# Optimization experiments

Hardware: AMD Instinct MI355X
Metric: run time of the kernel (lower is better)

## Reference

```python
import jax, jax.numpy as jnp
import numpy as np

ALPHA = 0.2  # LeakyReLU negative slope
NEG_INF = -9e15


def setup_inputs() -> dict:
    key = jax.random.key(0)
    k1, k2, k3, k4 = jax.random.split(key, 4)
    N, F_IN, F_OUT = 8192, 128, 64
    h = jax.random.normal(k1, (N, F_IN), dtype=jnp.float32)
    adj = jax.random.randint(k2, (N, N), 0, 2, dtype=jnp.int32)
    # xavier_uniform with gain=1.414 (as in the torch module)
    gain = 1.414
    bW = gain * np.sqrt(6.0 / (F_IN + F_OUT))
    W = jax.random.uniform(k3, (F_IN, F_OUT), dtype=jnp.float32, minval=-bW, maxval=bW)
    ba = gain * np.sqrt(6.0 / (2 * F_OUT + 1))
    a = jax.random.uniform(k4, (2 * F_OUT, 1), dtype=jnp.float32, minval=-ba, maxval=ba)
    return {"h": h, "adj": adj, "W": W, "a": a}


def reference(h, adj, W, a):
    # Wh: [N, F_out]
    Wh = h @ W
    F_out = Wh.shape[1]
    # Decompose a^T [Wh_i || Wh_j] = (Wh @ a_src)_i + (Wh @ a_dst)_j
    # (same math as the repeat+concat construction, without the N*N*2F tensor)
    src = Wh @ a[:F_out, 0]   # [N]
    dst = Wh @ a[F_out:, 0]   # [N]
    e = jax.nn.leaky_relu(src[:, None] + dst[None, :], negative_slope=ALPHA)  # [N, N]
    e = jnp.where(adj > 0, e, jnp.float32(NEG_INF))
    attention = jax.nn.softmax(e, axis=1)  # [N, N]
    h_prime = attention @ Wh               # [N, F_out]
    return jax.nn.elu(h_prime)
```

## Files before the change

### kernel.cpp

```cpp
#include <hip/hip_runtime.h>

#define ALPHA 0.2f
#define NN 8192
#define FIN 128
#define FOUT 64

typedef short bf16x8 __attribute__((ext_vector_type(8)));
typedef float f32x4 __attribute__((ext_vector_type(4)));

__device__ __forceinline__ unsigned short f2b(float x) {
    unsigned u = __builtin_bit_cast(unsigned, x);
    unsigned r = (u + 0x7fffu + ((u >> 16) & 1u)) >> 16;
    return (unsigned short)r;
}

__global__ __launch_bounds__(256) void gat_k0(const int* __restrict__ adj,
                                              unsigned long long* __restrict__ adjb) {
    int t = threadIdx.x, w = t >> 6, l = t & 63;
    int row = blockIdx.x * 4 + w;
    const int4* a4 = (const int4*)(adj + (size_t)row * NN);
    unsigned long long* ob = adjb + (size_t)row * 32 * 4;
#pragma unroll 4
    for (int it = 0; it < 32; ++it) {
        int4 av = a4[it * 64 + l];
        unsigned long long b0 = __ballot(av.x != 0);
        unsigned long long b1 = __ballot(av.y != 0);
        unsigned long long b2 = __ballot(av.z != 0);
        unsigned long long b3 = __ballot(av.w != 0);
        if (l == 0) {
            ulonglong4 v;
            v.x = b0; v.y = b1; v.z = b2; v.w = b3;
            *(ulonglong4*)(ob + it * 4) = v;
        }
    }
}

__global__ __launch_bounds__(256) void gat_k1(const float* __restrict__ h,
                                              const float* __restrict__ W,
                                              const float* __restrict__ a,
                                              float* __restrict__ Wh,
                                              float* __restrict__ src,
                                              float* __restrict__ dst) {
    __shared__ float wlds[FIN * FOUT];
    int t = threadIdx.x;
    const float4* W4 = (const float4*)W;
    float4* wlds4 = (float4*)wlds;
#pragma unroll
    for (int q = 0; q < 8; ++q) wlds4[q * 256 + t] = W4[q * 256 + t];
    __syncthreads();
    int wave = t >> 6, lane = t & 63;
    int row = blockIdx.x * 4 + wave;
    const float4* h4 = (const float4*)(h + (size_t)row * FIN);
    float acc = 0.f;
#pragma unroll
    for (int k4 = 0; k4 < 32; ++k4) {
        float4 hv = h4[k4];
        acc = fmaf(hv.x, wlds[(k4 * 4 + 0) * 64 + lane], acc);
        acc = fmaf(hv.y, wlds[(k4 * 4 + 1) * 64 + lane], acc);
        acc = fmaf(hv.z, wlds[(k4 * 4 + 2) * 64 + lane], acc);
        acc = fmaf(hv.w, wlds[(k4 * 4 + 3) * 64 + lane], acc);
    }
    Wh[(size_t)row * 64 + lane] = acc;
    float sa = acc * a[lane];
    float da = acc * a[64 + lane];
#pragma unroll
    for (int off = 32; off; off >>= 1) {
        sa += __shfl_xor(sa, off);
        da += __shfl_xor(da, off);
    }
    if (lane == 0) { src[row] = sa; dst[row] = da; }
}

__global__ __launch_bounds__(256) void gat_k1b(const float* __restrict__ Wh,
                                               unsigned short* __restrict__ whbt) {
    __shared__ unsigned short t16[64 * 68];
    int t = threadIdx.x;
    int rb = blockIdx.x * 64;
    const float4* s4 = (const float4*)(Wh + (size_t)rb * 64);
#pragma unroll
    for (int q = 0; q < 4; ++q) {
        float4 v = s4[t * 4 + q];
        int flat = t * 16 + q * 4;
        int r = flat >> 6, f = flat & 63;
        unsigned short* p = &t16[r * 68 + f];
        p[0] = f2b(v.x); p[1] = f2b(v.y); p[2] = f2b(v.z); p[3] = f2b(v.w);
    }
    __syncthreads();
    int f = t >> 2, qr = t & 3;
    unsigned v[8];
#pragma unroll
    for (int k = 0; k < 8; ++k) {
        unsigned lo = t16[(qr * 16 + 2 * k + 0) * 68 + f];
        unsigned hi = t16[(qr * 16 + 2 * k + 1) * 68 + f];
        v[k] = lo | (hi << 16);
    }
    uint4* o = (uint4*)(whbt + (size_t)f * NN + rb + qr * 16);
    o[0] = make_uint4(v[0], v[1], v[2], v[3]);
    o[1] = make_uint4(v[4], v[5], v[6], v[7]);
}

__global__ __launch_bounds__(256) void gat_k2(const unsigned long long* __restrict__ adjb,
                                              const unsigned short* __restrict__ whbt,
                                              const float* __restrict__ src,
                                              const float* __restrict__ dst,
                                              float* __restrict__ pl,
                                              float* __restrict__ pacc,
                                              int ns, int js) {
    const int l = threadIdx.x & 63;
    const int w = threadIdx.x >> 6;
    const int r = l & 15;
    const int g = l >> 4;
    const int s = blockIdx.x;
    const int rg = blockIdx.y;
    const int task = rg * ns + s;
    const int row = rg * 64 + w * 16 + r;
    const int j0 = s * js;

    const float srcv = src[row];
    const float4* dst4 = (const float4*)dst;
    const unsigned long long* brow = adjb + (size_t)row * 32 * 4;

    f32x4 acc0 = {0.f, 0.f, 0.f, 0.f}, acc1 = acc0, acc2 = acc0, acc3 = acc0, accl = acc0;
    bf16x8 bones;
#pragma unroll
    for (int e = 0; e < 8; ++e) bones[e] = (short)0x3F80;

    const int g0 = j0 >> 8, g1 = (j0 + js) >> 8;
    ulonglong2 mA = *(const ulonglong2*)(brow + g0 * 4);
    ulonglong2 mB = *(const ulonglong2*)(brow + g0 * 4 + 2);

    for (int grp = g0; grp < g1; ++grp) {
        int ng = (grp + 1 < g1) ? grp + 1 : g0;
        ulonglong2 nA = *(const ulonglong2*)(brow + ng * 4);
        ulonglong2 nB = *(const ulonglong2*)(brow + ng * 4 + 2);
        unsigned long long m0 = mA.x, m1 = mA.y, m2 = mB.x, m3 = mB.y;
        const int jgrp = grp << 8;
#pragma unroll 2
        for (int hh = 0; hh < 8; ++hh) {
            const int jh = jgrp + hh * 32;
            const int hb = hh * 8 + 2 * g;
            float4 d0 = dst4[(jh >> 2) + 2 * g];
            float4 d1 = dst4[(jh >> 2) + 2 * g + 1];
            float xs[8] = {d0.x, d0.y, d0.z, d0.w, d1.x, d1.y, d1.z, d1.w};
            float p[8];
#pragma unroll
            for (int e = 0; e < 8; ++e) {
                float x = srcv + xs[e];
                float lr = fmaxf(x, 0.f) + ALPHA * fminf(x, 0.f);
                float pe = __expf(lr);
                unsigned long long mm = (e & 3) == 0 ? m0 : (e & 3) == 1 ? m1
                                      : (e & 3) == 2 ? m2 : m3;
                unsigned bit = (unsigned)(mm >> (hb + (e >> 2))) & 1u;
                p[e] = bit ? pe : 0.f;
            }
            unsigned pw0, pw1, pw2, pw3;
            asm("v_cvt_pk_bf16_f32 %0, %1, %2" : "=v"(pw0) : "v"(p[0]), "v"(p[1]));
            asm("v_cvt_pk_bf16_f32 %0, %1, %2" : "=v"(pw1) : "v"(p[2]), "v"(p[3]));
            asm("v_cvt_pk_bf16_f32 %0, %1, %2" : "=v"(pw2) : "v"(p[4]), "v"(p[5]));
            asm("v_cvt_pk_bf16_f32 %0, %1, %2" : "=v"(pw3) : "v"(p[6]), "v"(p[7]));
            uint4 pwv = make_uint4(pw0, pw1, pw2, pw3);
            bf16x8 af = __builtin_bit_cast(bf16x8, pwv);

            const unsigned short* bbase = whbt + (size_t)r * NN + jh + 8 * g;
            bf16x8 b0 = *(const bf16x8*)(bbase + 0 * 16 * NN);
            bf16x8 b1 = *(const bf16x8*)(bbase + 1 * 16 * NN);
            bf16x8 b2 = *(const bf16x8*)(bbase + 2 * 16 * NN);
            bf16x8 b3 = *(const bf16x8*)(bbase + 3 * 16 * NN);
            acc0 = __builtin_amdgcn_mfma_f32_16x16x32_bf16(af, b0, acc0, 0, 0, 0);
            acc1 = __builtin_amdgcn_mfma_f32_16x16x32_bf16(af, b1, acc1, 0, 0, 0);
            acc2 = __builtin_amdgcn_mfma_f32_16x16x32_bf16(af, b2, acc2, 0, 0, 0);
            acc3 = __builtin_amdgcn_mfma_f32_16x16x32_bf16(af, b3, acc3, 0, 0, 0);
            accl = __builtin_amdgcn_mfma_f32_16x16x32_bf16(af, bones, accl, 0, 0, 0);
        }
        mA = nA; mB = nB;
    }

    if (r == 0) {
        float* plo = pl + (size_t)task * 64 + w * 16 + g * 4;
        plo[0] = accl[0]; plo[1] = accl[1]; plo[2] = accl[2]; plo[3] = accl[3];
    }

    float* po = pacc + (size_t)task * 4096 + (size_t)(w * 16) * 64;
#pragma unroll
    for (int reg = 0; reg < 4; ++reg) {
        int m = g * 4 + reg;
        po[m * 64 + 0 * 16 + r] = acc0[reg];
        po[m * 64 + 1 * 16 + r] = acc1[reg];
        po[m * 64 + 2 * 16 + r] = acc2[reg];
        po[m * 64 + 3 * 16 + r] = acc3[reg];
    }
}

__global__ __launch_bounds__(256) void gat_k3(const float* __restrict__ pl,
                                              const float* __restrict__ pacc,
                                              float* __restrict__ out, int ns) {
    int t = threadIdx.x;
    int wave = t >> 6, lane = t & 63;
    int row = blockIdx.x * 4 + wave;
    int rg = row >> 6, rr = row & 63;
    float L = 0.f, o = 0.f;
    for (int s2 = 0; s2 < ns; ++s2) {
        L += pl[(size_t)(rg * ns + s2) * 64 + rr];
        o += pacc[(size_t)(rg * ns + s2) * 4096 + rr * 64 + lane];
    }
    float hp = o / L;
    out[(size_t)row * 64 + lane] = hp > 0.f ? hp : __expf(hp) - 1.f;
}

extern "C" void kernel_launch(void* const* d_in, const int* in_sizes, int n_in,
                              void* d_out, int out_size, void* d_ws, size_t ws_size,
                              hipStream_t stream) {
    const float* h = (const float*)d_in[0];
    const int* adj = (const int*)d_in[1];
    const float* W = (const float*)d_in[2];
    const float* a = (const float*)d_in[3];
    float* out = (float*)d_out;
    float* ws = (float*)d_ws;

    size_t avail = ws_size / sizeof(float);
    int ns = 4;
    while (ns > 1 && (size_t)2899968 + (size_t)ns * 532480 > avail) ns >>= 1;
    int js = NN / ns;

    float* Wh = ws;
    float* src = Wh + (size_t)NN * FOUT;
    float* dst = src + NN;
    float* pl = dst + NN;
    float* pacc = pl + (size_t)128 * ns * 64;
    unsigned short* whbt = (unsigned short*)(pacc + (size_t)128 * ns * 4096);
    unsigned long long* adjb = (unsigned long long*)((float*)whbt + 262144);

    gat_k0<<<dim3(NN / 4), dim3(256), 0, stream>>>(adj, adjb);
    gat_k1<<<dim3(NN / 4), dim3(256), 0, stream>>>(h, W, a, Wh, src, dst);
    gat_k1b<<<dim3(NN / 64), dim3(256), 0, stream>>>(Wh, whbt);
    gat_k2<<<dim3(ns, 128), dim3(256), 0, stream>>>(adjb, whbt, src, dst, pl, pacc, ns, js);
    gat_k3<<<dim3(NN / 4), dim3(256), 0, stream>>>(pl, pacc, out, ns);
}
```

Before: 455.2 us.

## Pre-swizzle bf16 Wh into MFMA fragment layout and prefetch in flattened loop

The Wh transpose kernel now writes bf16 values in the exact per-lane MFMA B-fragment order, so the attention kernel makes one coalesced 16-byte load per lane per step instead of four strided row loads. The main loop is flattened to one 32-column step per iteration and software-prefetches the next step's B fragments and adjacency mask words. The column split count is raised from 4 to 8, and occupancy hints are added. In exchange, the partial-result buffers and the final reduction grow, and register pressure from prefetching rises.

```diff
diff --git a/kernel.cpp b/kernel.cpp
--- a/kernel.cpp
+++ b/kernel.cpp
@@ -7,12 +7,6 @@
 
 typedef short bf16x8 __attribute__((ext_vector_type(8)));
 typedef float f32x4 __attribute__((ext_vector_type(4)));
-
-__device__ __forceinline__ unsigned short f2b(float x) {
-    unsigned u = __builtin_bit_cast(unsigned, x);
-    unsigned r = (u + 0x7fffu + ((u >> 16) & 1u)) >> 16;
-    return (unsigned short)r;
-}
 
 __global__ __launch_bounds__(256) void gat_k0(const int* __restrict__ adj,
                                               unsigned long long* __restrict__ adjb) {
@@ -72,40 +66,33 @@
 }
 
 __global__ __launch_bounds__(256) void gat_k1b(const float* __restrict__ Wh,
-                                               unsigned short* __restrict__ whbt) {
-    __shared__ unsigned short t16[64 * 68];
-    int t = threadIdx.x;
-    int rb = blockIdx.x * 64;
-    const float4* s4 = (const float4*)(Wh + (size_t)rb * 64);
-#pragma unroll
-    for (int q = 0; q < 4; ++q) {
-        float4 v = s4[t * 4 + q];
-        int flat = t * 16 + q * 4;
-        int r = flat >> 6, f = flat & 63;
-        unsigned short* p = &t16[r * 68 + f];
-        p[0] = f2b(v.x); p[1] = f2b(v.y); p[2] = f2b(v.z); p[3] = f2b(v.w);
-    }
+                                               uint4* __restrict__ whbt2) {
+    __shared__ float wt[32 * 64];
+    int tid = threadIdx.x;
+    int t = blockIdx.x;
+    const float4* s4 = (const float4*)(Wh + (size_t)t * 2048);
+    float4* l4 = (float4*)wt;
+    l4[tid] = s4[tid];
+    l4[tid + 256] = s4[tid + 256];
     __syncthreads();
-    int f = t >> 2, qr = t & 3;
-    unsigned v[8];
-#pragma unroll
-    for (int k = 0; k < 8; ++k) {
-        unsigned lo = t16[(qr * 16 + 2 * k + 0) * 68 + f];
-        unsigned hi = t16[(qr * 16 + 2 * k + 1) * 68 + f];
-        v[k] = lo | (hi << 16);
-    }
-    uint4* o = (uint4*)(whbt + (size_t)f * NN + rb + qr * 16);
-    o[0] = make_uint4(v[0], v[1], v[2], v[3]);
-    o[1] = make_uint4(v[4], v[5], v[6], v[7]);
-}
-
-__global__ __launch_bounds__(256) void gat_k2(const unsigned long long* __restrict__ adjb,
-                                              const unsigned short* __restrict__ whbt,
-                                              const float* __restrict__ src,
-                                              const float* __restrict__ dst,
-                                              float* __restrict__ pl,
-                                              float* __restrict__ pacc,
-                                              int ns, int js) {
+    int q = tid >> 6, l = tid & 63, r = l & 15, g = l >> 4;
+    unsigned pk[4];
+#pragma unroll
+    for (int k = 0; k < 4; ++k) {
+        float lo = wt[(8 * g + 2 * k + 0) * 64 + 16 * q + r];
+        float hi = wt[(8 * g + 2 * k + 1) * 64 + 16 * q + r];
+        asm("v_cvt_pk_bf16_f32 %0, %1, %2" : "=v"(pk[k]) : "v"(lo), "v"(hi));
+    }
+    whbt2[(size_t)t * 256 + tid] = make_uint4(pk[0], pk[1], pk[2], pk[3]);
+}
+
+__global__ __launch_bounds__(256, 4) void gat_k2(const unsigned long long* __restrict__ adjb,
+                                                 const uint4* __restrict__ whbt2,
+                                                 const float* __restrict__ src,
+                                                 const float* __restrict__ dst,
+                                                 float* __restrict__ pl,
+                                                 float* __restrict__ pacc,
+                                                 int ns, int js) {
     const int l = threadIdx.x & 63;
     const int w = threadIdx.x >> 6;
     const int r = l & 15;
@@ -115,34 +102,43 @@
     const int task = rg * ns + s;
     const int row = rg * 64 + w * 16 + r;
     const int j0 = s * js;
+    const int steps = js >> 5;
 
     const float srcv = src[row];
     const float4* dst4 = (const float4*)dst;
-    const unsigned long long* brow = adjb + (size_t)row * 32 * 4;
+    const ulonglong2* brow2 = (const ulonglong2*)(adjb + (size_t)row * 128);
+    const uint4* bt = whbt2 + l;
 
     f32x4 acc0 = {0.f, 0.f, 0.f, 0.f}, acc1 = acc0, acc2 = acc0, acc3 = acc0, accl = acc0;
     bf16x8 bones;
 #pragma unroll
     for (int e = 0; e < 8; ++e) bones[e] = (short)0x3F80;
 
-    const int g0 = j0 >> 8, g1 = (j0 + js) >> 8;
-    ulonglong2 mA = *(const ulonglong2*)(brow + g0 * 4);
-    ulonglong2 mB = *(const ulonglong2*)(brow + g0 * 4 + 2);
-
-    for (int grp = g0; grp < g1; ++grp) {
-        int ng = (grp + 1 < g1) ? grp + 1 : g0;
-        ulonglong2 nA = *(const ulonglong2*)(brow + ng * 4);
-        ulonglong2 nB = *(const ulonglong2*)(brow + ng * 4 + 2);
-        unsigned long long m0 = mA.x, m1 = mA.y, m2 = mB.x, m3 = mB.y;
-        const int jgrp = grp << 8;
-#pragma unroll 2
-        for (int hh = 0; hh < 8; ++hh) {
-            const int jh = jgrp + hh * 32;
-            const int hb = hh * 8 + 2 * g;
-            float4 d0 = dst4[(jh >> 2) + 2 * g];
-            float4 d1 = dst4[(jh >> 2) + 2 * g + 1];
+    int jh = j0;
+    uint4 b0 = bt[(jh >> 5) * 256 + 0 * 64];
+    uint4 b1 = bt[(jh >> 5) * 256 + 1 * 64];
+    uint4 b2 = bt[(jh >> 5) * 256 + 2 * 64];
+    uint4 b3 = bt[(jh >> 5) * 256 + 3 * 64];
+    ulonglong2 mA = brow2[(jh >> 8) * 2 + 0];
+    ulonglong2 mB = brow2[(jh >> 8) * 2 + 1];
+
+    for (int t = 0; t < steps; ++t, jh += 32) {
+        const int jn = (t + 1 < steps) ? jh + 32 : j0;
+        uint4 nb0 = bt[(jn >> 5) * 256 + 0 * 64];
+        uint4 nb1 = bt[(jn >> 5) * 256 + 1 * 64];
+        uint4 nb2 = bt[(jn >> 5) * 256 + 2 * 64];
+        uint4 nb3 = bt[(jn >> 5) * 256 + 3 * 64];
+        ulonglong2 nmA = brow2[(jn >> 8) * 2 + 0];
+        ulonglong2 nmB = brow2[(jn >> 8) * 2 + 1];
+
+        float4 d0 = dst4[(jh >> 2) + 2 * g];
+        float4 d1 = dst4[(jh >> 2) + 2 * g + 1];
+        const int hb = ((jh >> 5) & 7) * 8 + 2 * g;
+        const unsigned long long m0 = mA.x, m1 = mA.y, m2 = mB.x, m3 = mB.y;
+
+        float p[8];
+        {
             float xs[8] = {d0.x, d0.y, d0.z, d0.w, d1.x, d1.y, d1.z, d1.w};
-            float p[8];
 #pragma unroll
             for (int e = 0; e < 8; ++e) {
                 float x = srcv + xs[e];
@@ -153,26 +149,22 @@
                 unsigned bit = (unsigned)(mm >> (hb + (e >> 2))) & 1u;
                 p[e] = bit ? pe : 0.f;
             }
-            unsigned pw0, pw1, pw2, pw3;
-            asm("v_cvt_pk_bf16_f32 %0, %1, %2" : "=v"(pw0) : "v"(p[0]), "v"(p[1]));
-            asm("v_cvt_pk_bf16_f32 %0, %1, %2" : "=v"(pw1) : "v"(p[2]), "v"(p[3]));
-            asm("v_cvt_pk_bf16_f32 %0, %1, %2" : "=v"(pw2) : "v"(p[4]), "v"(p[5]));
-            asm("v_cvt_pk_bf16_f32 %0, %1, %2" : "=v"(pw3) : "v"(p[6]), "v"(p[7]));
-            uint4 pwv = make_uint4(pw0, pw1, pw2, pw3);
-            bf16x8 af = __builtin_bit_cast(bf16x8, pwv);
-
-            const unsigned short* bbase = whbt + (size_t)r * NN + jh + 8 * g;
-            bf16x8 b0 = *(const bf16x8*)(bbase + 0 * 16 * NN);
-            bf16x8 b1 = *(const bf16x8*)(bbase + 1 * 16 * NN);
-            bf16x8 b2 = *(const bf16x8*)(bbase + 2 * 16 * NN);
-            bf16x8 b3 = *(const bf16x8*)(bbase + 3 * 16 * NN);
-            acc0 = __builtin_amdgcn_mfma_f32_16x16x32_bf16(af, b0, acc0, 0, 0, 0);
-            acc1 = __builtin_amdgcn_mfma_f32_16x16x32_bf16(af, b1, acc1, 0, 0, 0);
-            acc2 = __builtin_amdgcn_mfma_f32_16x16x32_bf16(af, b2, acc2, 0, 0, 0);
-            acc3 = __builtin_amdgcn_mfma_f32_16x16x32_bf16(af, b3, acc3, 0, 0, 0);
-            accl = __builtin_amdgcn_mfma_f32_16x16x32_bf16(af, bones, accl, 0, 0, 0);
         }
-        mA = nA; mB = nB;
+        unsigned pw0, pw1, pw2, pw3;
+        asm("v_cvt_pk_bf16_f32 %0, %1, %2" : "=v"(pw0) : "v"(p[0]), "v"(p[1]));
+        asm("v_cvt_pk_bf16_f32 %0, %1, %2" : "=v"(pw1) : "v"(p[2]), "v"(p[3]));
+        asm("v_cvt_pk_bf16_f32 %0, %1, %2" : "=v"(pw2) : "v"(p[4]), "v"(p[5]));
+        asm("v_cvt_pk_bf16_f32 %0, %1, %2" : "=v"(pw3) : "v"(p[6]), "v"(p[7]));
+        bf16x8 af = __builtin_bit_cast(bf16x8, make_uint4(pw0, pw1, pw2, pw3));
+
+        acc0 = __builtin_amdgcn_mfma_f32_16x16x32_bf16(af, __builtin_bit_cast(bf16x8, b0), acc0, 0, 0, 0);
+        acc1 = __builtin_amdgcn_mfma_f32_16x16x32_bf16(af, __builtin_bit_cast(bf16x8, b1), acc1, 0, 0, 0);
+        acc2 = __builtin_amdgcn_mfma_f32_16x16x32_bf16(af, __builtin_bit_cast(bf16x8, b2), acc2, 0, 0, 0);
+        acc3 = __builtin_amdgcn_mfma_f32_16x16x32_bf16(af, __builtin_bit_cast(bf16x8, b3), acc3, 0, 0, 0);
+        accl = __builtin_amdgcn_mfma_f32_16x16x32_bf16(af, bones, accl, 0, 0, 0);
+
+        b0 = nb0; b1 = nb1; b2 = nb2; b3 = nb3;
+        mA = nmA; mB = nmB;
     }
 
     if (r == 0) {
@@ -218,7 +210,7 @@
     float* ws = (float*)d_ws;
 
     size_t avail = ws_size / sizeof(float);
-    int ns = 4;
+    int ns = 8;
     while (ns > 1 && (size_t)2899968 + (size_t)ns * 532480 > avail) ns >>= 1;
     int js = NN / ns;
 
@@ -227,12 +219,12 @@
     float* dst = src + NN;
     float* pl = dst + NN;
     float* pacc = pl + (size_t)128 * ns * 64;
-    unsigned short* whbt = (unsigned short*)(pacc + (size_t)128 * ns * 4096);
-    unsigned long long* adjb = (unsigned long long*)((float*)whbt + 262144);
+    uint4* whbt2 = (uint4*)(pacc + (size_t)128 * ns * 4096);
+    unsigned long long* adjb = (unsigned long long*)((float*)whbt2 + 262144);
 
     gat_k0<<<dim3(NN / 4), dim3(256), 0, stream>>>(adj, adjb);
     gat_k1<<<dim3(NN / 4), dim3(256), 0, stream>>>(h, W, a, Wh, src, dst);
-    gat_k1b<<<dim3(NN / 64), dim3(256), 0, stream>>>(Wh, whbt);
-    gat_k2<<<dim3(ns, 128), dim3(256), 0, stream>>>(adjb, whbt, src, dst, pl, pacc, ns, js);
+    gat_k1b<<<dim3(NN / 32), dim3(256), 0, stream>>>(Wh, whbt2);
+    gat_k2<<<dim3(ns, 128), dim3(256), 0, stream>>>(adjb, whbt2, src, dst, pl, pacc, ns, js);
     gat_k3<<<dim3(NN / 4), dim3(256), 0, stream>>>(pl, pacc, out, ns);
 }
```

New measurement: 445.9 us. 1.02x faster.
